# Optimization experiments

Measured on AMD Instinct MI355X. Metric: run time of the kernel, lower is better.

The kernel has to match this reference:

```python
import jax, jax.numpy as jnp
import numpy as np

N = 2048      # nodes
E = 65536     # edges (avg degree 32)
NV = 6        # n_views (edge_attr dim)
C1, C2, C3 = 32, 32, 32


def _nnconv(x, edge_index, edge_attr, W, b, root, bias, in_c, out_c):
    # Edge MLP: Linear(n_views, in*out) + ReLU -> per-edge weight matrix [E, in, out]
    w = jax.nn.relu(edge_attr @ W + b).reshape(-1, in_c, out_c)
    src, dst = edge_index[0], edge_index[1]  # source_to_target flow
    msg = jnp.einsum('ei,eio->eo', x[src], w)          # gather + edge-specific matmul
    summed = jax.ops.segment_sum(msg, dst, num_segments=N)
    cnt = jax.ops.segment_sum(jnp.ones((msg.shape[0],), x.dtype), dst, num_segments=N)
    agg = summed / jnp.maximum(cnt, 1.0)[:, None]       # scatter-mean (0 for isolated nodes)
    return agg + x @ root + bias                        # root weight + bias (PyG NNConv defaults)


def setup_inputs() -> dict:
    key = jax.random.key(0)
    ks = jax.random.split(key, 12)
    s = 0.1
    return {
        'x': jax.random.normal(ks[0], (N, 1), jnp.float32),
        'edge_attr': jax.random.uniform(ks[1], (E, NV), jnp.float32),
        'edge_index': jax.random.randint(ks[2], (2, E), 0, N, jnp.int64),
        'W1': jax.random.normal(ks[3], (NV, 1 * C1), jnp.float32) * s,
        'b1': jnp.zeros((1 * C1,), jnp.float32),
        'root1': jax.random.normal(ks[4], (1, C1), jnp.float32) * s,
        'bias1': jnp.zeros((C1,), jnp.float32),
        'W2': jax.random.normal(ks[5], (NV, C1 * C2), jnp.float32) * s,
        'b2': jnp.zeros((C1 * C2,), jnp.float32),
        'root2': jax.random.normal(ks[6], (C1, C2), jnp.float32) * s,
        'bias2': jnp.zeros((C2,), jnp.float32),
        'W3': jax.random.normal(ks[7], (NV, C2 * C3), jnp.float32) * s,
        'b3': jnp.zeros((C2 * C3,), jnp.float32),
        'root3': jax.random.normal(ks[8], (C2, C3), jnp.float32) * s,
        'bias3': jnp.zeros((C3,), jnp.float32),
    }


def reference(x, edge_attr, edge_index, W1, b1, root1, bias1, W2, b2, root2, bias2, W3, b3, root3, bias3):
    h = jax.nn.relu(_nnconv(x, edge_index, edge_attr, W1, b1, root1, bias1, 1, C1))
    h = jax.nn.relu(_nnconv(h, edge_index, edge_attr, W2, b2, root2, bias2, C1, C2))
    h = jax.nn.relu(_nnconv(h, edge_index, edge_attr, W3, b3, root3, bias3, C2, C3))
    # CBT: cbt[i, j] = sum_k |h[j, k] - h[i, k]|  (all-pairs L1 distance, [N, N])
    cbt = jnp.sum(jnp.abs(h[None, :, :] - h[:, None, :]), axis=2)
    return cbt
```

## Files before the change

### kernel.cpp

```cpp
#include <hip/hip_runtime.h>

#define N_NODES 2048
#define N_EDGES 65536
#define NV 6
#define C 32


__global__ void edge1_kernel(const float* __restrict__ x,
                             const float* __restrict__ ea,
                             const int* __restrict__ src,
                             const int* __restrict__ dst,
                             const float* __restrict__ W1,
                             const float* __restrict__ b1,
                             float* __restrict__ sum1,
                             float* __restrict__ cnt) {
    int t = blockIdx.x * blockDim.x + threadIdx.x;
    int e = t >> 5, o = t & 31;
    if (e >= N_EDGES) return;
    const float* eap = ea + e * NV;
    float w = b1[o];
#pragma unroll
    for (int v = 0; v < NV; v++) w = fmaf(eap[v], W1[v * C + o], w);
    w = fmaxf(w, 0.0f);
    int d = dst[e];
    atomicAdd(&sum1[d * C + o], x[src[e]] * w);
    if (o == 0) atomicAdd(&cnt[d], 1.0f);
}

template <int IN_C>
__global__ void node_kernel(const float* __restrict__ sum,
                            const float* __restrict__ cnt,
                            const float* __restrict__ hprev,
                            const float* __restrict__ root,
                            const float* __restrict__ bias,
                            float* __restrict__ hout) {
    int t = blockIdx.x * blockDim.x + threadIdx.x;
    int n = t >> 5, o = t & 31;
    float inv = 1.0f / fmaxf(cnt[n], 1.0f);
    float acc = sum[t] * inv + bias[o];
#pragma unroll
    for (int i = 0; i < IN_C; i++) acc = fmaf(hprev[n * IN_C + i], root[i * C + o], acc);
    hout[t] = fmaxf(acc, 0.0f);
}

__global__ __launch_bounds__(256, 4) void edge23_kernel(
    const float* __restrict__ hprev,
    const float* __restrict__ ea,
    const int* __restrict__ src,
    const int* __restrict__ dst,
    const float* __restrict__ W,
    const float* __restrict__ b,
    float* __restrict__ sumout)
{
    __shared__ float Wall[6 * 1024];
    __shared__ float hb[4][256];
    for (int i = threadIdx.x; i < 6 * 1024; i += 256) Wall[i] = W[i];
    __syncthreads();

    const int lane = threadIdx.x & 63;
    const int o = lane & 31;
    const int half = lane >> 5;
    const int i0 = half * 16;
    const int w = threadIdx.x >> 6;
    const int g = (blockIdx.x * 256 + threadIdx.x) >> 6;
    const int e0 = g * 8;
    float* hbw = &hb[w][0];

    float breg[16];
#pragma unroll
    for (int j = 0; j < 16; j++) breg[j] = b[(i0 + j) * C + o];

    float eaf[48];
    const float4* eap4 = (const float4*)(ea + (size_t)e0 * NV);
#pragma unroll
    for (int t = 0; t < 12; t++) *(float4*)&eaf[t * 4] = eap4[t];

    const int4 sq = *(const int4*)&src[e0 + half * 4];
    float4 hq;
    hq.x = hprev[sq.x * C + o];
    hq.y = hprev[sq.y * C + o];
    hq.z = hprev[sq.z * C + o];
    hq.w = hprev[sq.w * C + o];
    *(float4*)&hbw[half * 128 + o * 4] = hq;

    float acc[8] = {0, 0, 0, 0, 0, 0, 0, 0};
#pragma unroll
    for (int j = 0; j < 16; j++) {
        const int idx = (i0 + j) * C + o;
        const float w0 = Wall[idx];
        const float w1 = Wall[1024 + idx];
        const float w2 = Wall[2048 + idx];
        const float w3 = Wall[3072 + idx];
        const float w4 = Wall[4096 + idx];
        const float w5 = Wall[5120 + idx];
        const float bb = breg[j];
        const float4 hA = *(const float4*)&hbw[(i0 + j) * 4];
        const float4 hB = *(const float4*)&hbw[128 + (i0 + j) * 4];
        const float hv[8] = {hA.x, hA.y, hA.z, hA.w, hB.x, hB.y, hB.z, hB.w};
#pragma unroll
        for (int k = 0; k < 8; k++) {
            const float* eap = &eaf[k * 6];
            float t = bb;
            t = fmaf(eap[0], w0, t);
            t = fmaf(eap[1], w1, t);
            t = fmaf(eap[2], w2, t);
            t = fmaf(eap[3], w3, t);
            t = fmaf(eap[4], w4, t);
            t = fmaf(eap[5], w5, t);
            acc[k] = fmaf(hv[k], fmaxf(t, 0.0f), acc[k]);
        }
    }
#pragma unroll
    for (int k = 0; k < 8; k++) acc[k] += __shfl_down(acc[k], 32);

    const int4 dA = *(const int4*)&dst[e0];
    const int4 dB = *(const int4*)&dst[e0 + 4];
    if (lane < 32) {
        atomicAdd(&sumout[dA.x * C + o], acc[0]);
        atomicAdd(&sumout[dA.y * C + o], acc[1]);
        atomicAdd(&sumout[dA.z * C + o], acc[2]);
        atomicAdd(&sumout[dA.w * C + o], acc[3]);
        atomicAdd(&sumout[dB.x * C + o], acc[4]);
        atomicAdd(&sumout[dB.y * C + o], acc[5]);
        atomicAdd(&sumout[dB.z * C + o], acc[6]);
        atomicAdd(&sumout[dB.w * C + o], acc[7]);
    }
}

__global__ __launch_bounds__(256) void cbt_kernel(const float* __restrict__ h,
                                                  float* __restrict__ out) {
    __shared__ float hj_s[64][33];
    __shared__ float hi_s[64 * 32];
    const int lane = threadIdx.x & 63;
    const int w = threadIdx.x >> 6;
    const int j0 = blockIdx.x * 64;
    const int i0 = blockIdx.y * 64;
    for (int t = threadIdx.x; t < 64 * 32; t += 256) {
        hj_s[t >> 5][t & 31] = h[j0 * 32 + t];
        hi_s[t] = h[i0 * 32 + t];
    }
    __syncthreads();
    float hj[32];
#pragma unroll
    for (int k = 0; k < 32; k++) hj[k] = hj_s[lane][k];
    const int j = j0 + lane;
#pragma unroll 4
    for (int ii = w * 16; ii < w * 16 + 16; ii++) {
        float acc = 0.0f;
#pragma unroll
        for (int k = 0; k < 32; k++) {
            acc += fabsf(hi_s[ii * 32 + k] - hj[k]);
        }
        out[(size_t)(i0 + ii) * N_NODES + j] = acc;
    }
}

extern "C" void kernel_launch(void* const* d_in, const int* in_sizes, int n_in,
                              void* d_out, int out_size, void* d_ws, size_t ws_size,
                              hipStream_t stream) {
    const float* x         = (const float*)d_in[0];
    const float* edge_attr = (const float*)d_in[1];
    const int*   edge_idx  = (const int*)d_in[2];
    const float* W1 = (const float*)d_in[3];
    const float* b1 = (const float*)d_in[4];
    const float* root1 = (const float*)d_in[5];
    const float* bias1 = (const float*)d_in[6];
    const float* W2 = (const float*)d_in[7];
    const float* b2 = (const float*)d_in[8];
    const float* root2 = (const float*)d_in[9];
    const float* bias2 = (const float*)d_in[10];
    const float* W3 = (const float*)d_in[11];
    const float* b3 = (const float*)d_in[12];
    const float* root3 = (const float*)d_in[13];
    const float* bias3 = (const float*)d_in[14];

    const int* src = edge_idx;
    const int* dst = edge_idx + N_EDGES;

    float* ws   = (float*)d_ws;
    float* cnt  = ws;
    float* sum1 = ws + N_NODES;
    float* sum2 = sum1 + N_NODES * C;
    float* sum3 = sum2 + N_NODES * C;
    float* h1   = sum3 + N_NODES * C;
    float* h2   = h1 + N_NODES * C;
    float* h3   = h2 + N_NODES * C;

    hipMemsetAsync(d_ws, 0, (size_t)(N_NODES + 3 * N_NODES * C) * sizeof(float), stream);

    edge1_kernel<<<(N_EDGES * C) / 256, 256, 0, stream>>>(x, edge_attr, src, dst, W1, b1, sum1, cnt);
    node_kernel<1><<<(N_NODES * C) / 256, 256, 0, stream>>>(sum1, cnt, x, root1, bias1, h1);

    edge23_kernel<<<2048, 256, 0, stream>>>(h1, edge_attr, src, dst, W2, b2, sum2);
    node_kernel<C><<<(N_NODES * C) / 256, 256, 0, stream>>>(sum2, cnt, h1, root2, bias2, h2);

    edge23_kernel<<<2048, 256, 0, stream>>>(h2, edge_attr, src, dst, W3, b3, sum3);
    node_kernel<C><<<(N_NODES * C) / 256, 256, 0, stream>>>(sum3, cnt, h2, root3, bias3, h3);

    cbt_kernel<<<dim3(N_NODES / 64, N_NODES / 64), 256, 0, stream>>>(h3, (float*)d_out);
}
```

Before: 169.4 us.

## Hold edge-MLP weights in registers and grid-stride edge23 over fewer blocks

Result: no change. 168.5 us (-0.5%).

```diff
diff --git a/kernel.cpp b/kernel.cpp
--- a/kernel.cpp
+++ b/kernel.cpp
@@ -43,7 +43,7 @@
     hout[t] = fmaxf(acc, 0.0f);
 }
 
-__global__ __launch_bounds__(256, 4) void edge23_kernel(
+__global__ __launch_bounds__(256) void edge23_kernel(
     const float* __restrict__ hprev,
     const float* __restrict__ ea,
     const int* __restrict__ src,
@@ -52,78 +52,83 @@
     const float* __restrict__ b,
     float* __restrict__ sumout)
 {
-    __shared__ float Wall[6 * 1024];
     __shared__ float hb[4][256];
-    for (int i = threadIdx.x; i < 6 * 1024; i += 256) Wall[i] = W[i];
-    __syncthreads();
-
     const int lane = threadIdx.x & 63;
     const int o = lane & 31;
     const int half = lane >> 5;
     const int i0 = half * 16;
     const int w = threadIdx.x >> 6;
-    const int g = (blockIdx.x * 256 + threadIdx.x) >> 6;
-    const int e0 = g * 8;
     float* hbw = &hb[w][0];
 
-    float breg[16];
-#pragma unroll
-    for (int j = 0; j < 16; j++) breg[j] = b[(i0 + j) * C + o];
-
-    float eaf[48];
-    const float4* eap4 = (const float4*)(ea + (size_t)e0 * NV);
-#pragma unroll
-    for (int t = 0; t < 12; t++) *(float4*)&eaf[t * 4] = eap4[t];
-
-    const int4 sq = *(const int4*)&src[e0 + half * 4];
-    float4 hq;
-    hq.x = hprev[sq.x * C + o];
-    hq.y = hprev[sq.y * C + o];
-    hq.z = hprev[sq.z * C + o];
-    hq.w = hprev[sq.w * C + o];
-    *(float4*)&hbw[half * 128 + o * 4] = hq;
-
-    float acc[8] = {0, 0, 0, 0, 0, 0, 0, 0};
+    float wreg[16][6], breg[16];
 #pragma unroll
     for (int j = 0; j < 16; j++) {
-        const int idx = (i0 + j) * C + o;
-        const float w0 = Wall[idx];
-        const float w1 = Wall[1024 + idx];
-        const float w2 = Wall[2048 + idx];
-        const float w3 = Wall[3072 + idx];
-        const float w4 = Wall[4096 + idx];
-        const float w5 = Wall[5120 + idx];
-        const float bb = breg[j];
-        const float4 hA = *(const float4*)&hbw[(i0 + j) * 4];
-        const float4 hB = *(const float4*)&hbw[128 + (i0 + j) * 4];
-        const float hv[8] = {hA.x, hA.y, hA.z, hA.w, hB.x, hB.y, hB.z, hB.w};
-#pragma unroll
-        for (int k = 0; k < 8; k++) {
-            const float* eap = &eaf[k * 6];
-            float t = bb;
-            t = fmaf(eap[0], w0, t);
-            t = fmaf(eap[1], w1, t);
-            t = fmaf(eap[2], w2, t);
-            t = fmaf(eap[3], w3, t);
-            t = fmaf(eap[4], w4, t);
-            t = fmaf(eap[5], w5, t);
-            acc[k] = fmaf(hv[k], fmaxf(t, 0.0f), acc[k]);
+#pragma unroll
+        for (int v = 0; v < 6; v++) wreg[j][v] = W[v * 1024 + (i0 + j) * C + o];
+        breg[j] = b[(i0 + j) * C + o];
+    }
+
+    const int wid = (blockIdx.x * 256 + threadIdx.x) >> 6;
+    for (int g = wid; g < N_EDGES / 8; g += 2048) {
+        const int e0 = g * 8;
+        const int4 sq = *(const int4*)&src[e0 + half * 4];
+        float4 hq;
+        hq.x = hprev[sq.x * C + o];
+        hq.y = hprev[sq.y * C + o];
+        hq.z = hprev[sq.z * C + o];
+        hq.w = hprev[sq.w * C + o];
+        *(float4*)&hbw[half * 128 + o * 4] = hq;
+
+        float accs[8];
+        const float4* eap4 = (const float4*)(ea + (size_t)e0 * NV);
+#pragma unroll
+        for (int sub = 0; sub < 2; sub++) {
+            float eaf[24];
+#pragma unroll
+            for (int t = 0; t < 6; t++) *(float4*)&eaf[t * 4] = eap4[sub * 6 + t];
+            float a0 = 0.0f, a1 = 0.0f, a2 = 0.0f, a3 = 0.0f;
+#pragma unroll
+            for (int j = 0; j < 16; j++) {
+                const float4 hA = *(const float4*)&hbw[sub * 128 + (i0 + j) * 4];
+                const float bb = breg[j];
+                const float w0 = wreg[j][0], w1 = wreg[j][1], w2 = wreg[j][2];
+                const float w3 = wreg[j][3], w4 = wreg[j][4], w5 = wreg[j][5];
+                float t0 = bb, t1 = bb, t2 = bb, t3 = bb;
+                t0 = fmaf(eaf[0],  w0, t0); t1 = fmaf(eaf[6],  w0, t1);
+                t2 = fmaf(eaf[12], w0, t2); t3 = fmaf(eaf[18], w0, t3);
+                t0 = fmaf(eaf[1],  w1, t0); t1 = fmaf(eaf[7],  w1, t1);
+                t2 = fmaf(eaf[13], w1, t2); t3 = fmaf(eaf[19], w1, t3);
+                t0 = fmaf(eaf[2],  w2, t0); t1 = fmaf(eaf[8],  w2, t1);
+                t2 = fmaf(eaf[14], w2, t2); t3 = fmaf(eaf[20], w2, t3);
+                t0 = fmaf(eaf[3],  w3, t0); t1 = fmaf(eaf[9],  w3, t1);
+                t2 = fmaf(eaf[15], w3, t2); t3 = fmaf(eaf[21], w3, t3);
+                t0 = fmaf(eaf[4],  w4, t0); t1 = fmaf(eaf[10], w4, t1);
+                t2 = fmaf(eaf[16], w4, t2); t3 = fmaf(eaf[22], w4, t3);
+                t0 = fmaf(eaf[5],  w5, t0); t1 = fmaf(eaf[11], w5, t1);
+                t2 = fmaf(eaf[17], w5, t2); t3 = fmaf(eaf[23], w5, t3);
+                a0 = fmaf(hA.x, fmaxf(t0, 0.0f), a0);
+                a1 = fmaf(hA.y, fmaxf(t1, 0.0f), a1);
+                a2 = fmaf(hA.z, fmaxf(t2, 0.0f), a2);
+                a3 = fmaf(hA.w, fmaxf(t3, 0.0f), a3);
+            }
+            accs[sub * 4 + 0] = a0; accs[sub * 4 + 1] = a1;
+            accs[sub * 4 + 2] = a2; accs[sub * 4 + 3] = a3;
         }
-    }
-#pragma unroll
-    for (int k = 0; k < 8; k++) acc[k] += __shfl_down(acc[k], 32);
-
-    const int4 dA = *(const int4*)&dst[e0];
-    const int4 dB = *(const int4*)&dst[e0 + 4];
-    if (lane < 32) {
-        atomicAdd(&sumout[dA.x * C + o], acc[0]);
-        atomicAdd(&sumout[dA.y * C + o], acc[1]);
-        atomicAdd(&sumout[dA.z * C + o], acc[2]);
-        atomicAdd(&sumout[dA.w * C + o], acc[3]);
-        atomicAdd(&sumout[dB.x * C + o], acc[4]);
-        atomicAdd(&sumout[dB.y * C + o], acc[5]);
-        atomicAdd(&sumout[dB.z * C + o], acc[6]);
-        atomicAdd(&sumout[dB.w * C + o], acc[7]);
+#pragma unroll
+        for (int k = 0; k < 8; k++) accs[k] += __shfl_down(accs[k], 32);
+
+        const int4 dA = *(const int4*)&dst[e0];
+        const int4 dB = *(const int4*)&dst[e0 + 4];
+        if (lane < 32) {
+            atomicAdd(&sumout[dA.x * C + o], accs[0]);
+            atomicAdd(&sumout[dA.y * C + o], accs[1]);
+            atomicAdd(&sumout[dA.z * C + o], accs[2]);
+            atomicAdd(&sumout[dA.w * C + o], accs[3]);
+            atomicAdd(&sumout[dB.x * C + o], accs[4]);
+            atomicAdd(&sumout[dB.y * C + o], accs[5]);
+            atomicAdd(&sumout[dB.z * C + o], accs[6]);
+            atomicAdd(&sumout[dB.w * C + o], accs[7]);
+        }
     }
 }
 
@@ -191,10 +196,10 @@
     edge1_kernel<<<(N_EDGES * C) / 256, 256, 0, stream>>>(x, edge_attr, src, dst, W1, b1, sum1, cnt);
     node_kernel<1><<<(N_NODES * C) / 256, 256, 0, stream>>>(sum1, cnt, x, root1, bias1, h1);
 
-    edge23_kernel<<<2048, 256, 0, stream>>>(h1, edge_attr, src, dst, W2, b2, sum2);
+    edge23_kernel<<<512, 256, 0, stream>>>(h1, edge_attr, src, dst, W2, b2, sum2);
     node_kernel<C><<<(N_NODES * C) / 256, 256, 0, stream>>>(sum2, cnt, h1, root2, bias2, h2);
 
-    edge23_kernel<<<2048, 256, 0, stream>>>(h2, edge_attr, src, dst, W3, b3, sum3);
+    edge23_kernel<<<512, 256, 0, stream>>>(h2, edge_attr, src, dst, W3, b3, sum3);
     node_kernel<C><<<(N_NODES * C) / 256, 256, 0, stream>>>(sum3, cnt, h2, root3, bias3, h3);
 
     cbt_kernel<<<dim3(N_NODES / 64, N_NODES / 64), 256, 0, stream>>>(h3, (float*)d_out);
```

## Fuse all stages into one cooperative persistent kernel with grid syncs

Applied to the files above, without the earlier changes.

After: 531.4 us. +213.7%, slower.

```diff
diff --git a/kernel.cpp b/kernel.cpp
--- a/kernel.cpp
+++ b/kernel.cpp
@@ -1,60 +1,74 @@
 #include <hip/hip_runtime.h>
+#include <hip/hip_cooperative_groups.h>
+
+namespace cg = cooperative_groups;
 
 #define N_NODES 2048
 #define N_EDGES 65536
 #define NV 6
 #define C 32
-
-
-__global__ void edge1_kernel(const float* __restrict__ x,
-                             const float* __restrict__ ea,
-                             const int* __restrict__ src,
-                             const int* __restrict__ dst,
-                             const float* __restrict__ W1,
-                             const float* __restrict__ b1,
-                             float* __restrict__ sum1,
-                             float* __restrict__ cnt) {
-    int t = blockIdx.x * blockDim.x + threadIdx.x;
-    int e = t >> 5, o = t & 31;
-    if (e >= N_EDGES) return;
-    const float* eap = ea + e * NV;
-    float w = b1[o];
-#pragma unroll
-    for (int v = 0; v < NV; v++) w = fmaf(eap[v], W1[v * C + o], w);
-    w = fmaxf(w, 0.0f);
-    int d = dst[e];
-    atomicAdd(&sum1[d * C + o], x[src[e]] * w);
-    if (o == 0) atomicAdd(&cnt[d], 1.0f);
+#define BLK 256
+
+
+struct MegaArgs {
+    const float* x; const float* ea; const int* src; const int* dst;
+    const float* W1; const float* b1; const float* root1; const float* bias1;
+    const float* W2; const float* b2; const float* root2; const float* bias2;
+    const float* W3; const float* b3; const float* root3; const float* bias3;
+    float* cnt; float* sum1; float* sum2; float* sum3;
+    float* h1; float* h2; float* h3; float* out;
+};
+
+union SharedU {
+    struct { float Wall[6 * 1024]; float hb[4][256]; } e23;
+    struct { float hj[64 * 33]; float hi[64 * 32]; } cbt;
+};
+
+__device__ __forceinline__ void zero_phase(float* __restrict__ cnt, int gtid, int nth) {
+    for (int i = gtid; i < N_NODES + 3 * N_NODES * C; i += nth) cnt[i] = 0.0f;
+}
+
+__device__ __forceinline__ void edge1_phase(const MegaArgs& a, int gtid, int nth) {
+    for (int t = gtid; t < N_EDGES * C; t += nth) {
+        const int e = t >> 5, o = t & 31;
+        const float* eap = a.ea + e * NV;
+        float wv = a.b1[o];
+#pragma unroll
+        for (int v = 0; v < NV; v++) wv = fmaf(eap[v], a.W1[v * C + o], wv);
+        wv = fmaxf(wv, 0.0f);
+        const int d = a.dst[e];
+        atomicAdd(&a.sum1[d * C + o], a.x[a.src[e]] * wv);
+        if (o == 0) atomicAdd(&a.cnt[d], 1.0f);
+    }
 }
 
 template <int IN_C>
-__global__ void node_kernel(const float* __restrict__ sum,
-                            const float* __restrict__ cnt,
-                            const float* __restrict__ hprev,
-                            const float* __restrict__ root,
-                            const float* __restrict__ bias,
-                            float* __restrict__ hout) {
-    int t = blockIdx.x * blockDim.x + threadIdx.x;
-    int n = t >> 5, o = t & 31;
-    float inv = 1.0f / fmaxf(cnt[n], 1.0f);
-    float acc = sum[t] * inv + bias[o];
-#pragma unroll
-    for (int i = 0; i < IN_C; i++) acc = fmaf(hprev[n * IN_C + i], root[i * C + o], acc);
-    hout[t] = fmaxf(acc, 0.0f);
-}
-
-__global__ __launch_bounds__(256, 4) void edge23_kernel(
-    const float* __restrict__ hprev,
-    const float* __restrict__ ea,
-    const int* __restrict__ src,
-    const int* __restrict__ dst,
-    const float* __restrict__ W,
-    const float* __restrict__ b,
-    float* __restrict__ sumout)
-{
-    __shared__ float Wall[6 * 1024];
-    __shared__ float hb[4][256];
-    for (int i = threadIdx.x; i < 6 * 1024; i += 256) Wall[i] = W[i];
+__device__ __forceinline__ void node_phase(const float* __restrict__ sum,
+                                           const float* __restrict__ cnt,
+                                           const float* __restrict__ hprev,
+                                           const float* __restrict__ root,
+                                           const float* __restrict__ bias,
+                                           float* __restrict__ hout, int gtid, int nth) {
+    for (int t = gtid; t < N_NODES * C; t += nth) {
+        const int n = t >> 5, o = t & 31;
+        const float inv = 1.0f / fmaxf(cnt[n], 1.0f);
+        float acc = fmaf(sum[t], inv, bias[o]);
+#pragma unroll
+        for (int i = 0; i < IN_C; i++) acc = fmaf(hprev[n * IN_C + i], root[i * C + o], acc);
+        hout[t] = fmaxf(acc, 0.0f);
+    }
+}
+
+__device__ __forceinline__ void edge23_phase(SharedU& sh,
+                                             const float* __restrict__ hprev,
+                                             const float* __restrict__ ea,
+                                             const int* __restrict__ src,
+                                             const int* __restrict__ dst,
+                                             const float* __restrict__ W,
+                                             const float* __restrict__ b,
+                                             float* __restrict__ sumout) {
+    float* Wall = sh.e23.Wall;
+    for (int i = threadIdx.x; i < 6 * 1024; i += BLK) Wall[i] = W[i];
     __syncthreads();
 
     const int lane = threadIdx.x & 63;
@@ -62,140 +76,193 @@
     const int half = lane >> 5;
     const int i0 = half * 16;
     const int w = threadIdx.x >> 6;
-    const int g = (blockIdx.x * 256 + threadIdx.x) >> 6;
-    const int e0 = g * 8;
-    float* hbw = &hb[w][0];
+    float* hbw = &sh.e23.hb[w][0];
 
     float breg[16];
 #pragma unroll
     for (int j = 0; j < 16; j++) breg[j] = b[(i0 + j) * C + o];
 
-    float eaf[48];
-    const float4* eap4 = (const float4*)(ea + (size_t)e0 * NV);
-#pragma unroll
-    for (int t = 0; t < 12; t++) *(float4*)&eaf[t * 4] = eap4[t];
-
-    const int4 sq = *(const int4*)&src[e0 + half * 4];
-    float4 hq;
-    hq.x = hprev[sq.x * C + o];
-    hq.y = hprev[sq.y * C + o];
-    hq.z = hprev[sq.z * C + o];
-    hq.w = hprev[sq.w * C + o];
-    *(float4*)&hbw[half * 128 + o * 4] = hq;
-
-    float acc[8] = {0, 0, 0, 0, 0, 0, 0, 0};
-#pragma unroll
-    for (int j = 0; j < 16; j++) {
-        const int idx = (i0 + j) * C + o;
-        const float w0 = Wall[idx];
-        const float w1 = Wall[1024 + idx];
-        const float w2 = Wall[2048 + idx];
-        const float w3 = Wall[3072 + idx];
-        const float w4 = Wall[4096 + idx];
-        const float w5 = Wall[5120 + idx];
-        const float bb = breg[j];
-        const float4 hA = *(const float4*)&hbw[(i0 + j) * 4];
-        const float4 hB = *(const float4*)&hbw[128 + (i0 + j) * 4];
-        const float hv[8] = {hA.x, hA.y, hA.z, hA.w, hB.x, hB.y, hB.z, hB.w};
-#pragma unroll
-        for (int k = 0; k < 8; k++) {
-            const float* eap = &eaf[k * 6];
-            float t = bb;
-            t = fmaf(eap[0], w0, t);
-            t = fmaf(eap[1], w1, t);
-            t = fmaf(eap[2], w2, t);
-            t = fmaf(eap[3], w3, t);
-            t = fmaf(eap[4], w4, t);
-            t = fmaf(eap[5], w5, t);
-            acc[k] = fmaf(hv[k], fmaxf(t, 0.0f), acc[k]);
-        }
-    }
-#pragma unroll
-    for (int k = 0; k < 8; k++) acc[k] += __shfl_down(acc[k], 32);
-
-    const int4 dA = *(const int4*)&dst[e0];
-    const int4 dB = *(const int4*)&dst[e0 + 4];
-    if (lane < 32) {
-        atomicAdd(&sumout[dA.x * C + o], acc[0]);
-        atomicAdd(&sumout[dA.y * C + o], acc[1]);
-        atomicAdd(&sumout[dA.z * C + o], acc[2]);
-        atomicAdd(&sumout[dA.w * C + o], acc[3]);
-        atomicAdd(&sumout[dB.x * C + o], acc[4]);
-        atomicAdd(&sumout[dB.y * C + o], acc[5]);
-        atomicAdd(&sumout[dB.z * C + o], acc[6]);
-        atomicAdd(&sumout[dB.w * C + o], acc[7]);
-    }
-}
-
-__global__ __launch_bounds__(256) void cbt_kernel(const float* __restrict__ h,
-                                                  float* __restrict__ out) {
-    __shared__ float hj_s[64][33];
-    __shared__ float hi_s[64 * 32];
+    const int nw = (gridDim.x * BLK) >> 6;
+    const int wid = (blockIdx.x * BLK + threadIdx.x) >> 6;
+    for (int g = wid; g < N_EDGES / 8; g += nw) {
+        const int e0 = g * 8;
+        float eaf[48];
+        const float4* eap4 = (const float4*)(ea + (size_t)e0 * NV);
+#pragma unroll
+        for (int t = 0; t < 12; t++) *(float4*)&eaf[t * 4] = eap4[t];
+
+        const int4 sq = *(const int4*)&src[e0 + half * 4];
+        float4 hq;
+        hq.x = hprev[sq.x * C + o];
+        hq.y = hprev[sq.y * C + o];
+        hq.z = hprev[sq.z * C + o];
+        hq.w = hprev[sq.w * C + o];
+        *(float4*)&hbw[half * 128 + o * 4] = hq;
+
+        float acc[8] = {0, 0, 0, 0, 0, 0, 0, 0};
+#pragma unroll
+        for (int j = 0; j < 16; j++) {
+            const int idx = (i0 + j) * C + o;
+            const float w0 = Wall[idx];
+            const float w1 = Wall[1024 + idx];
+            const float w2 = Wall[2048 + idx];
+            const float w3 = Wall[3072 + idx];
+            const float w4 = Wall[4096 + idx];
+            const float w5 = Wall[5120 + idx];
+            const float bb = breg[j];
+            const float4 hA = *(const float4*)&hbw[(i0 + j) * 4];
+            const float4 hB = *(const float4*)&hbw[128 + (i0 + j) * 4];
+            const float hv[8] = {hA.x, hA.y, hA.z, hA.w, hB.x, hB.y, hB.z, hB.w};
+#pragma unroll
+            for (int k = 0; k < 8; k++) {
+                const float* eap = &eaf[k * 6];
+                float t = bb;
+                t = fmaf(eap[0], w0, t);
+                t = fmaf(eap[1], w1, t);
+                t = fmaf(eap[2], w2, t);
+                t = fmaf(eap[3], w3, t);
+                t = fmaf(eap[4], w4, t);
+                t = fmaf(eap[5], w5, t);
+                acc[k] = fmaf(hv[k], fmaxf(t, 0.0f), acc[k]);
+            }
+        }
+#pragma unroll
+        for (int k = 0; k < 8; k++) acc[k] += __shfl_down(acc[k], 32);
+
+        const int4 dA = *(const int4*)&dst[e0];
+        const int4 dB = *(const int4*)&dst[e0 + 4];
+        if (lane < 32) {
+            atomicAdd(&sumout[dA.x * C + o], acc[0]);
+            atomicAdd(&sumout[dA.y * C + o], acc[1]);
+            atomicAdd(&sumout[dA.z * C + o], acc[2]);
+            atomicAdd(&sumout[dA.w * C + o], acc[3]);
+            atomicAdd(&sumout[dB.x * C + o], acc[4]);
+            atomicAdd(&sumout[dB.y * C + o], acc[5]);
+            atomicAdd(&sumout[dB.z * C + o], acc[6]);
+            atomicAdd(&sumout[dB.w * C + o], acc[7]);
+        }
+    }
+}
+
+__device__ __forceinline__ void cbt_phase(SharedU& sh, const float* __restrict__ h,
+                                          float* __restrict__ out) {
     const int lane = threadIdx.x & 63;
     const int w = threadIdx.x >> 6;
-    const int j0 = blockIdx.x * 64;
-    const int i0 = blockIdx.y * 64;
-    for (int t = threadIdx.x; t < 64 * 32; t += 256) {
-        hj_s[t >> 5][t & 31] = h[j0 * 32 + t];
-        hi_s[t] = h[i0 * 32 + t];
-    }
-    __syncthreads();
-    float hj[32];
-#pragma unroll
-    for (int k = 0; k < 32; k++) hj[k] = hj_s[lane][k];
-    const int j = j0 + lane;
+    for (int T = blockIdx.x; T < 1024; T += gridDim.x) {
+        const int j0 = (T & 31) * 64;
+        const int i0 = (T >> 5) * 64;
+        __syncthreads();
+        for (int t = threadIdx.x; t < 64 * 32; t += BLK) {
+            sh.cbt.hj[(t >> 5) * 33 + (t & 31)] = h[j0 * 32 + t];
+            sh.cbt.hi[t] = h[i0 * 32 + t];
+        }
+        __syncthreads();
+        float hjr[32];
+#pragma unroll
+        for (int k = 0; k < 32; k++) hjr[k] = sh.cbt.hj[lane * 33 + k];
+        const int j = j0 + lane;
 #pragma unroll 4
-    for (int ii = w * 16; ii < w * 16 + 16; ii++) {
-        float acc = 0.0f;
-#pragma unroll
-        for (int k = 0; k < 32; k++) {
-            acc += fabsf(hi_s[ii * 32 + k] - hj[k]);
-        }
-        out[(size_t)(i0 + ii) * N_NODES + j] = acc;
-    }
+        for (int ii = w * 16; ii < w * 16 + 16; ii++) {
+            float acc = 0.0f;
+#pragma unroll
+            for (int k = 0; k < 32; k++) acc += fabsf(sh.cbt.hi[ii * 32 + k] - hjr[k]);
+            out[(size_t)(i0 + ii) * N_NODES + j] = acc;
+        }
+    }
+}
+
+__global__ __launch_bounds__(BLK, 2) void mega_kernel(MegaArgs a) {
+    __shared__ SharedU sh;
+    cg::grid_group grid = cg::this_grid();
+    const int nth = gridDim.x * BLK;
+    const int gtid = blockIdx.x * BLK + threadIdx.x;
+
+    zero_phase(a.cnt, gtid, nth);
+    grid.sync();
+    edge1_phase(a, gtid, nth);
+    grid.sync();
+    node_phase<1>(a.sum1, a.cnt, a.x, a.root1, a.bias1, a.h1, gtid, nth);
+    grid.sync();
+    edge23_phase(sh, a.h1, a.ea, a.src, a.dst, a.W2, a.b2, a.sum2);
+    grid.sync();
+    node_phase<C>(a.sum2, a.cnt, a.h1, a.root2, a.bias2, a.h2, gtid, nth);
+    grid.sync();
+    edge23_phase(sh, a.h2, a.ea, a.src, a.dst, a.W3, a.b3, a.sum3);
+    grid.sync();
+    node_phase<C>(a.sum3, a.cnt, a.h2, a.root3, a.bias3, a.h3, gtid, nth);
+    grid.sync();
+    cbt_phase(sh, a.h3, a.out);
+}
+
+__global__ __launch_bounds__(BLK) void k_edge1(MegaArgs a) {
+    edge1_phase(a, blockIdx.x * BLK + threadIdx.x, gridDim.x * BLK);
+}
+template <int IN_C>
+__global__ __launch_bounds__(BLK) void k_node(const float* sum, const float* cnt,
+                                              const float* hprev, const float* root,
+                                              const float* bias, float* hout) {
+    node_phase<IN_C>(sum, cnt, hprev, root, bias, hout,
+                     blockIdx.x * BLK + threadIdx.x, gridDim.x * BLK);
+}
+__global__ __launch_bounds__(BLK) void k_edge23(MegaArgs a, const float* hprev,
+                                                const float* W, const float* b,
+                                                float* sumout) {
+    __shared__ SharedU sh;
+    edge23_phase(sh, hprev, a.ea, a.src, a.dst, W, b, sumout);
+}
+__global__ __launch_bounds__(BLK) void k_cbt(const float* h, float* out) {
+    __shared__ SharedU sh;
+    cbt_phase(sh, h, out);
 }
 
 extern "C" void kernel_launch(void* const* d_in, const int* in_sizes, int n_in,
                               void* d_out, int out_size, void* d_ws, size_t ws_size,
                               hipStream_t stream) {
-    const float* x         = (const float*)d_in[0];
-    const float* edge_attr = (const float*)d_in[1];
-    const int*   edge_idx  = (const int*)d_in[2];
-    const float* W1 = (const float*)d_in[3];
-    const float* b1 = (const float*)d_in[4];
-    const float* root1 = (const float*)d_in[5];
-    const float* bias1 = (const float*)d_in[6];
-    const float* W2 = (const float*)d_in[7];
-    const float* b2 = (const float*)d_in[8];
-    const float* root2 = (const float*)d_in[9];
-    const float* bias2 = (const float*)d_in[10];
-    const float* W3 = (const float*)d_in[11];
-    const float* b3 = (const float*)d_in[12];
-    const float* root3 = (const float*)d_in[13];
-    const float* bias3 = (const float*)d_in[14];
-
-    const int* src = edge_idx;
-    const int* dst = edge_idx + N_EDGES;
-
-    float* ws   = (float*)d_ws;
-    float* cnt  = ws;
-    float* sum1 = ws + N_NODES;
-    float* sum2 = sum1 + N_NODES * C;
-    float* sum3 = sum2 + N_NODES * C;
-    float* h1   = sum3 + N_NODES * C;
-    float* h2   = h1 + N_NODES * C;
-    float* h3   = h2 + N_NODES * C;
-
-    hipMemsetAsync(d_ws, 0, (size_t)(N_NODES + 3 * N_NODES * C) * sizeof(float), stream);
-
-    edge1_kernel<<<(N_EDGES * C) / 256, 256, 0, stream>>>(x, edge_attr, src, dst, W1, b1, sum1, cnt);
-    node_kernel<1><<<(N_NODES * C) / 256, 256, 0, stream>>>(sum1, cnt, x, root1, bias1, h1);
-
-    edge23_kernel<<<2048, 256, 0, stream>>>(h1, edge_attr, src, dst, W2, b2, sum2);
-    node_kernel<C><<<(N_NODES * C) / 256, 256, 0, stream>>>(sum2, cnt, h1, root2, bias2, h2);
-
-    edge23_kernel<<<2048, 256, 0, stream>>>(h2, edge_attr, src, dst, W3, b3, sum3);
-    node_kernel<C><<<(N_NODES * C) / 256, 256, 0, stream>>>(sum3, cnt, h2, root3, bias3, h3);
-
-    cbt_kernel<<<dim3(N_NODES / 64, N_NODES / 64), 256, 0, stream>>>(h3, (float*)d_out);
-}
+    float* ws = (float*)d_ws;
+    MegaArgs a;
+    a.x     = (const float*)d_in[0];
+    a.ea    = (const float*)d_in[1];
+    a.src   = (const int*)d_in[2];
+    a.dst   = (const int*)d_in[2] + N_EDGES;
+    a.W1    = (const float*)d_in[3];
+    a.b1    = (const float*)d_in[4];
+    a.root1 = (const float*)d_in[5];
+    a.bias1 = (const float*)d_in[6];
+    a.W2    = (const float*)d_in[7];
+    a.b2    = (const float*)d_in[8];
+    a.root2 = (const float*)d_in[9];
+    a.bias2 = (const float*)d_in[10];
+    a.W3    = (const float*)d_in[11];
+    a.b3    = (const float*)d_in[12];
+    a.root3 = (const float*)d_in[13];
+    a.bias3 = (const float*)d_in[14];
+    a.cnt  = ws;
+    a.sum1 = ws + N_NODES;
+    a.sum2 = a.sum1 + N_NODES * C;
+    a.sum3 = a.sum2 + N_NODES * C;
+    a.h1   = a.sum3 + N_NODES * C;
+    a.h2   = a.h1 + N_NODES * C;
+    a.h3   = a.h2 + N_NODES * C;
+    a.out  = (float*)d_out;
+
+    void* kp[] = {&a};
+    hipError_t err = hipLaunchCooperativeKernel((const void*)mega_kernel,
+                                                dim3(512), dim3(BLK), kp, 0, stream);
+    if (err != hipSuccess) {
+        (void)hipGetLastError();
+        err = hipLaunchCooperativeKernel((const void*)mega_kernel,
+                                         dim3(256), dim3(BLK), kp, 0, stream);
+    }
+    if (err != hipSuccess) {
+        (void)hipGetLastError();
+        hipMemsetAsync(d_ws, 0,
+                       (size_t)(N_NODES + 3 * N_NODES * C) * sizeof(float), stream);
+        k_edge1<<<(N_EDGES * C) / BLK, BLK, 0, stream>>>(a);
+        k_node<1><<<(N_NODES * C) / BLK, BLK, 0, stream>>>(a.sum1, a.cnt, a.x, a.root1, a.bias1, a.h1);
+        k_edge23<<<512, BLK, 0, stream>>>(a, a.h1, a.W2, a.b2, a.sum2);
+        k_node<C><<<(N_NODES * C) / BLK, BLK, 0, stream>>>(a.sum2, a.cnt, a.h1, a.root2, a.bias2, a.h2);
+        k_edge23<<<512, BLK, 0, stream>>>(a, a.h2, a.W3, a.b3, a.sum3);
+        k_node<C><<<(N_NODES * C) / BLK, BLK, 0, stream>>>(a.sum3, a.cnt, a.h2, a.root3, a.bias3, a.h3);
+        k_cbt<<<512, BLK, 0, stream>>>(a.h3, a.out);
+    }
+}
```
